# Performance work log

Measured on AMD Instinct MI355X. Metric: run time of the kernel, lower is better.

The kernel has to match this reference:

```python
import jax, jax.numpy as jnp
import numpy as np

B, S, D = 2, 2048, 2048
H, KVH, DH = 16, 4, 128
EPS = 1e-6
ROPE_BASE = 10000.0


def _rms_norm(x, eps=EPS):
    # weightless RMSNorm over the last (head) dim
    return x * jax.lax.rsqrt(jnp.mean(jnp.square(x), axis=-1, keepdims=True) + eps)


def _rope(x):
    # x: [b, s, h, d]; standard half-split RoPE, base 10000
    d = x.shape[-1]
    s = x.shape[1]
    inv_freq = 1.0 / (ROPE_BASE ** (jnp.arange(0, d // 2, dtype=jnp.float32) * 2.0 / d))
    ang = jnp.arange(s, dtype=jnp.float32)[:, None] * inv_freq[None, :]  # [s, d/2]
    cos = jnp.cos(ang)[None, :, None, :]
    sin = jnp.sin(ang)[None, :, None, :]
    x1, x2 = jnp.split(x, 2, axis=-1)
    return jnp.concatenate([x1 * cos - x2 * sin, x1 * sin + x2 * cos], axis=-1)


def setup_inputs() -> dict:
    key = jax.random.key(0)
    ks = jax.random.split(key, 5)
    x = jax.random.normal(ks[0], (B, S, D), dtype=jnp.float32)
    mask = jnp.tril(jnp.ones((S, S), dtype=bool))  # causal
    # eqx.Linear-style weights: [out, in], scaled init
    wq = jax.random.normal(ks[1], (D, D), dtype=jnp.float32) / np.sqrt(D)
    wk = jax.random.normal(ks[2], (KVH * DH, D), dtype=jnp.float32) / np.sqrt(D)
    wv = jax.random.normal(ks[3], (KVH * DH, D), dtype=jnp.float32) / np.sqrt(D)
    wo = jax.random.normal(ks[4], (D, D), dtype=jnp.float32) / np.sqrt(D)
    return {"x": x, "mask": mask, "wq": wq, "wk": wk, "wv": wv, "wo": wo}


def reference(x, mask, wq, wk, wv, wo):
    b, s, _ = x.shape
    q = jnp.einsum('bsi,oi->bso', x, wq).reshape(b, s, H, DH)
    k = jnp.einsum('bsi,oi->bso', x, wk).reshape(b, s, KVH, DH)
    v = jnp.einsum('bsi,oi->bso', x, wv).reshape(b, s, KVH, DH)
    rep = H // KVH
    k = jnp.repeat(k, rep, axis=-2)  # [b, s, H, DH]
    v = jnp.repeat(v, rep, axis=-2)
    q = _rms_norm(q)
    k = _rms_norm(k)
    q = _rope(q)
    k = _rope(k)
    scores = jnp.einsum('bshd,bthd->bhst', q, k) / jnp.sqrt(jnp.float32(DH))
    scores = jnp.where(mask[None, None], scores, -jnp.inf)
    w = jax.nn.softmax(scores, axis=-1)
    out = jnp.einsum('bhst,bthd->bshd', w, v).reshape(b, s, D)
    return jnp.einsum('bsi,oi->bso', out, wo)
```

## Files before the change

### kernel.cpp

```cpp
#include <hip/hip_runtime.h>
#include <hip/hip_bf16.h>

typedef unsigned short u16;
typedef unsigned int   u32;
typedef unsigned long long u64;
typedef __attribute__((ext_vector_type(8))) short bf16x8;
typedef __attribute__((ext_vector_type(4))) float f32x4;
typedef __attribute__((ext_vector_type(16))) float f32x16;

#define MFMA16(a,b,c) __builtin_amdgcn_mfma_f32_16x16x32_bf16((a),(b),(c),0,0,0)
#define MFMA32(a,b,c) __builtin_amdgcn_mfma_f32_32x32x16_bf16((a),(b),(c),0,0,0)

#define GLD16(gp, lp) __builtin_amdgcn_global_load_lds( \
    (const __attribute__((address_space(1))) void*)(gp), \
    (__attribute__((address_space(3))) void*)(lp), 16, 0, 0)

__device__ inline u32 pkbf(float a, float b) {
  __hip_bfloat16 ha = __float2bfloat16(a), hb = __float2bfloat16(b);
  return (u32)(*(u16*)&ha) | ((u32)(*(u16*)&hb) << 16);
}
__device__ inline float b2f(u16 x) {
  __hip_bfloat16 h; *(u16*)&h = x; return __bfloat162float(h);
}
__device__ inline u32 pk2(float a, float b) {
  u32 ua = __builtin_bit_cast(u32, a) + 0x8000u;
  u32 ub = __builtin_bit_cast(u32, b) + 0x8000u;
  return __builtin_amdgcn_perm(ub, ua, 0x07060302u);
}
__device__ inline float fmax3(float a, float b, float c) {
  return fmaxf(fmaxf(a, b), c);
}

__global__ __launch_bounds__(256) void cast_f32_bf16(const float* __restrict__ src,
                                                     u16* __restrict__ dst, int n4) {
  int i = blockIdx.x * 256 + threadIdx.x;
  if (i >= n4) return;
  float4 v = reinterpret_cast<const float4*>(src)[i];
  uint2 pk; pk.x = pkbf(v.x, v.y); pk.y = pkbf(v.z, v.w);
  reinterpret_cast<uint2*>(dst)[i] = pk;
}

__device__ inline void cstore(u16* C, size_t i, float v) {
  __hip_bfloat16 h = __float2bfloat16(v); C[i] = *(u16*)&h;
}
__device__ inline void cstore(float* C, size_t i, float v) { C[i] = v; }

template<typename OutT>
__global__ __launch_bounds__(512, 4) void gemm_big(const u16* __restrict__ A,
                                                   const u16* __restrict__ B,
                                                   OutT* __restrict__ C,
                                                   int M, int N, int K) {
  __shared__ u16 As[2][128 * 32];
  __shared__ u16 Bs[2][256 * 32];

  const int t = threadIdx.x;
  const int lane = t & 63, wid = t >> 6;
  const int l15 = lane & 15, l4 = lane >> 4;
  const int wr = wid >> 2, wc = wid & 3;

  const int nwg = gridDim.x * gridDim.y;
  int lid = blockIdx.y * gridDim.x + blockIdx.x;
  lid = (lid & 7) * (nwg >> 3) + (lid >> 3);
  const int m0 = (lid / gridDim.x) * 128, n0 = (lid % gridDim.x) * 256;

  const int ra = t >> 2;
  const int ca = (t & 3) ^ ((ra >> 1) & 3);
  const u16* Ag  = A + (size_t)(m0 + ra) * K + ca * 8;
  const u16* Bg0 = B + (size_t)(n0 + ra) * K + ca * 8;
  const u16* Bg1 = B + (size_t)(n0 + 128 + ra) * K + ca * 8;

#define STAGE(k0_, buf_) do {                                                 \
    GLD16(Ag  + (k0_), &As[buf_][t * 8]);                                     \
    GLD16(Bg0 + (k0_), &Bs[buf_][t * 8]);                                     \
    GLD16(Bg1 + (k0_), &Bs[buf_][4096 + t * 8]);                              \
  } while (0)

  const int nk = K >> 5;
  const int ks = (l15 >> 1) & 3;
  const int coff = ((l4 ^ ks) << 3);

  f32x4 acc[4][4] = {};

  STAGE(0, 0);
  STAGE(32, 1);

  for (int j = 0; j < nk; ++j) {
    const int cur = j & 1;
    if (j + 1 < nk) asm volatile("s_waitcnt vmcnt(3)" ::: "memory");
    else            asm volatile("s_waitcnt vmcnt(0)" ::: "memory");
    __builtin_amdgcn_s_barrier();
    __builtin_amdgcn_sched_barrier(0);

    bf16x8 af[4], bfr[4];
#pragma unroll
    for (int mi = 0; mi < 4; ++mi)
      af[mi] = *(const bf16x8*)&As[cur][(wr * 64 + mi * 16 + l15) * 32 + coff];
#pragma unroll
    for (int ni = 0; ni < 4; ++ni)
      bfr[ni] = *(const bf16x8*)&Bs[cur][(wc * 64 + ni * 16 + l15) * 32 + coff];
    __builtin_amdgcn_s_setprio(1);
#pragma unroll
    for (int mi = 0; mi < 4; ++mi)
#pragma unroll
      for (int ni = 0; ni < 4; ++ni)
        acc[mi][ni] = MFMA16(af[mi], bfr[ni], acc[mi][ni]);
    __builtin_amdgcn_s_setprio(0);

    __builtin_amdgcn_s_barrier();
    if (j + 2 < nk) STAGE((j + 2) << 5, cur);
  }

  const int crow = m0 + wr * 64 + (l4 << 2);
  const int ccol = n0 + wc * 64 + l15;
#pragma unroll
  for (int mi = 0; mi < 4; ++mi)
#pragma unroll
    for (int ni = 0; ni < 4; ++ni)
#pragma unroll
      for (int r = 0; r < 4; ++r)
        cstore(C, (size_t)(crow + mi * 16 + r) * N + (ccol + ni * 16), acc[mi][ni][r]);
#undef STAGE
}

__global__ __launch_bounds__(256) void rmsrope_kernel(u16* __restrict__ qkv) {
  const int t = threadIdx.x;
  const int lane = t & 63;
  const int gw = blockIdx.x * 4 + (t >> 6);
  const int row = gw / 20;
  const int hd = gw - row * 20;
  const int col = (hd < 16) ? hd * 128 : 2048 + (hd - 16) * 128;
  const size_t base = (size_t)row * 3072 + col;
  float x1 = b2f(qkv[base + lane]);
  float x2 = b2f(qkv[base + 64 + lane]);
  float ss = x1 * x1 + x2 * x2;
#pragma unroll
  for (int off = 32; off >= 1; off >>= 1) ss += __shfl_xor(ss, off, 64);
  const float qsc = (hd < 16) ? (0.08838834764831845f * 1.44269504088896340f)
                              : 1.0f;
  const float sc = rsqrtf(ss * (1.0f / 128.0f) + 1e-6f) * qsc;
  const int pos = row & 2047;
  const float inv_freq = exp2f(-(float)lane * (13.287712379549449f / 64.0f));
  float sn, cs;
  sincosf((float)pos * inv_freq, &sn, &cs);
  const float a = x1 * sc, b2 = x2 * sc;
  __hip_bfloat16 o1 = __float2bfloat16(a * cs - b2 * sn);
  __hip_bfloat16 o2 = __float2bfloat16(a * sn + b2 * cs);
  qkv[base + lane] = *(u16*)&o1;
  qkv[base + 64 + lane] = *(u16*)&o2;
}

__global__ __launch_bounds__(256) void vtrans_kernel(const u16* __restrict__ qkv,
                                                     u16* __restrict__ vt) {
  __shared__ u16 Ls[64 * 130];
  const int t = threadIdx.x;
  const int g = blockIdx.x & 7, sb = blockIdx.x >> 3;
  const int b = g >> 2, kvh = g & 3;
  const int vcol = 2560 + kvh * 128;
  {
    const int row = t >> 4, dch = t & 15;
    const u16* src = qkv + (size_t)(b * 2048 + sb * 64 + row) * 3072 + vcol + dch * 8;
#pragma unroll
    for (int it = 0; it < 4; ++it) {
      bf16x8 v = *(const bf16x8*)(src + (size_t)it * 16 * 3072);
      *(bf16x8*)&Ls[(row + it * 16) * 130 + dch * 8] = v;
    }
  }
  __syncthreads();
  const int c = t & 7, d0 = t >> 3;
  const int k0 = 4 * (8 * (c >> 2) + 4 * ((c >> 1) & 1) + (c & 1));
#pragma unroll
  for (int it = 0; it < 4; ++it) {
    const int d = d0 + 32 * it;
    u16 v[8];
#pragma unroll
    for (int e = 0; e < 8; ++e)
      v[e] = Ls[(k0 + (e & 3) + 8 * (e >> 2)) * 130 + d];
    u64 lo = (u64)v[0] | ((u64)v[1] << 16) | ((u64)v[2] << 32) | ((u64)v[3] << 48);
    u64 hi = (u64)v[4] | ((u64)v[5] << 16) | ((u64)v[6] << 32) | ((u64)v[7] << 48);
    u64* dst = (u64*)(vt + ((size_t)g * 128 + d) * 2048 + sb * 64 + c * 8);
    dst[0] = lo; dst[1] = hi;
  }
}

__global__ __launch_bounds__(256, 2) void attn_kernel(const u16* __restrict__ qkv,
                                                      const u16* __restrict__ vt,
                                                      u16* __restrict__ ao) {
  __shared__ u16 Ks[2][64 * 128];
  __shared__ u16 Vt[2][128 * 64];

  const int t = threadIdx.x;
  const int lane = t & 63, w = t >> 6;
  const int l31 = lane & 31, hi = lane >> 5;
  const int qg = w >> 1, hi2 = w & 1;

  const int bid = blockIdx.x;
  const int g = bid & 7;
  const int b = g >> 2, kvh = g & 3;
  const int idx = bid >> 3;
  const int h = kvh * 4 + (idx & 3);
  const int j = idx >> 2;

  const int kcol = 2048 + kvh * 128;
  const u16* vtg = vt + (size_t)g * 128 * 2048;

  const int krow_s = t >> 4, kchk = t & 15;
  const int vd = t >> 3, vc = t & 7;

#define STAGE_K(kb_, buf_) do {                                               \
    const size_t rb_ = (size_t)(b * 2048 + (kb_) * 64);                       \
    _Pragma("unroll")                                                         \
    for (int j_ = 0; j_ < 4; ++j_) {                                          \
      const int row_ = j_ * 16 + krow_s;                                      \
      GLD16(qkv + (rb_ + row_) * 3072 + kcol + ((kchk ^ (row_ & 7)) << 3),    \
            &Ks[buf_][(j_ * 256 + t) << 3]);                                  \
    } } while (0)

#define STAGE_V(kb_, buf_) do {                                               \
    _Pragma("unroll")                                                         \
    for (int j_ = 0; j_ < 4; ++j_) {                                          \
      const int d_ = j_ * 32 + vd;                                            \
      GLD16(vtg + (size_t)d_ * 2048 + (kb_) * 64 + ((vc ^ (d_ & 7)) << 3),    \
            &Vt[buf_][(j_ * 256 + t) << 3]);                                  \
    } } while (0)

  for (int ph = 0; ph < 2; ++ph) {
    const int qt64 = ph ? (31 - j) : j;
    const int q0 = qt64 * 64;
    const int nt = qt64 + 1;
    const int qrow = q0 + 32 * qg + l31;

    bf16x8 qf[8];
    {
      const u16* qp = qkv + (size_t)(b * 2048 + qrow) * 3072 + h * 128 + hi * 8;
#pragma unroll
      for (int st = 0; st < 8; ++st) qf[st] = *(const bf16x8*)(qp + st * 16);
    }

    f32x16 o[4];
#pragma unroll
    for (int dt = 0; dt < 4; ++dt)
#pragma unroll
      for (int i = 0; i < 16; ++i) o[dt][i] = 0.f;
    float m2 = -1e30f, l = 0.f;

    STAGE_K(0, 0);
    STAGE_V(0, 0);
    if (nt > 1) { STAGE_K(1, 1); STAGE_V(1, 1); }

    for (int kb = 0; kb < nt; ++kb) {
      const int cur = kb & 1;
      if (kb + 1 < nt) asm volatile("s_waitcnt vmcnt(8)" ::: "memory");
      else             asm volatile("s_waitcnt vmcnt(0)" ::: "memory");
      __builtin_amdgcn_s_barrier();
      __builtin_amdgcn_sched_barrier(0);

      f32x16 s;
#pragma unroll
      for (int i = 0; i < 16; ++i) s[i] = 0.f;
      const int kbase = (32 * hi2 + l31) * 128;
      const int ksw = l31 & 7;
      __builtin_amdgcn_s_setprio(1);
#pragma unroll
      for (int st = 0; st < 8; ++st) {
        bf16x8 ka = *(const bf16x8*)&Ks[cur][kbase + (((2 * st + hi) ^ ksw) << 3)];
        s = MFMA32(ka, qf[st], s);
      }
      __builtin_amdgcn_s_setprio(0);

      const bool nomask = (kb < qt64) || (hi2 == 0 && qg == 1);
      if (!nomask) {
#pragma unroll
        for (int i = 0; i < 16; ++i) {
          const int kr = kb * 64 + 32 * hi2 + (i & 3) + 8 * (i >> 2) + 4 * hi;
          s[i] = (kr <= qrow) ? s[i] : -INFINITY;
        }
      }
      float a0 = fmax3(s[0], s[1], s[2]);
      float a1 = fmax3(s[3], s[4], s[5]);
      float a2 = fmax3(s[6], s[7], s[8]);
      float a3 = fmax3(s[9], s[10], s[11]);
      float a4 = fmax3(s[12], s[13], s[14]);
      float b0 = fmax3(a0, a1, s[15]);
      float b1 = fmax3(a2, a3, a4);
      float pm = fmaxf(b0, b1);
      pm = fmaxf(pm, __shfl_xor(pm, 32));
      if (!__all(pm <= m2 + 8.f)) {
        const float m2n = fmaxf(m2, pm);
        const float fc = exp2f(m2 - m2n);
        m2 = m2n; l *= fc;
#pragma unroll
        for (int dt = 0; dt < 4; ++dt)
#pragma unroll
          for (int i = 0; i < 16; ++i) o[dt][i] *= fc;
      }
#pragma unroll
      for (int i = 0; i < 16; ++i) s[i] = exp2f(s[i] - m2);
      float t8[8];
#pragma unroll
      for (int i = 0; i < 8; ++i) t8[i] = s[i] + s[i + 8];
#pragma unroll
      for (int i = 0; i < 4; ++i) t8[i] = t8[i] + t8[i + 4];
      l += (t8[0] + t8[1]) + (t8[2] + t8[3]);
      union PB { u32 wd[4]; bf16x8 v; } p0u, p1u;
#pragma unroll
      for (int q_ = 0; q_ < 4; ++q_) {
        p0u.wd[q_] = pk2(s[2 * q_],     s[2 * q_ + 1]);
        p1u.wd[q_] = pk2(s[8 + 2 * q_], s[8 + 2 * q_ + 1]);
      }
      __builtin_amdgcn_s_setprio(1);
#pragma unroll
      for (int dt = 0; dt < 4; ++dt) {
        const int vrow = (dt * 32 + l31) * 64;
        const int dsw = l31 & 7;
        bf16x8 va0 = *(const bf16x8*)&Vt[cur][vrow + (((4 * hi2 + hi) ^ dsw) << 3)];
        o[dt] = MFMA32(va0, p0u.v, o[dt]);
        bf16x8 va1 = *(const bf16x8*)&Vt[cur][vrow + (((4 * hi2 + 2 + hi) ^ dsw) << 3)];
        o[dt] = MFMA32(va1, p1u.v, o[dt]);
      }
      __builtin_amdgcn_s_setprio(0);

      __builtin_amdgcn_s_barrier();
      if (kb + 2 < nt) { STAGE_K(kb + 2, cur); STAGE_V(kb + 2, cur); }
    }

    __syncthreads();
    const float l_tot = l + __shfl_xor(l, 32);
    float* Mrg = (float*)&Ks[0][0];
    float* Mlb = (float*)&Vt[0][0];
    const int sw8 = l31 & 7;
    if (hi2) {
#pragma unroll
      for (int dt = 0; dt < 4; ++dt) {
        const int rbase = ((qg * 4 + dt) * 32 + l31) * 32;
#pragma unroll
        for (int m_ = 0; m_ < 4; ++m_) {
          f32x4 cv;
          cv[0] = o[dt][4 * m_ + 0]; cv[1] = o[dt][4 * m_ + 1];
          cv[2] = o[dt][4 * m_ + 2]; cv[3] = o[dt][4 * m_ + 3];
          *(f32x4*)&Mrg[rbase + (((hi * 4 + m_) ^ sw8) << 2)] = cv;
        }
      }
      if (hi == 0) {
        Mlb[qg * 64 + l31] = m2;
        Mlb[qg * 64 + 32 + l31] = l_tot;
      }
    }
    __syncthreads();
    if (!hi2) {
      const float m1 = Mlb[qg * 64 + l31];
      const float l1 = Mlb[qg * 64 + 32 + l31];
      const float ms = fmaxf(m2, m1);
      const float w0 = exp2f(m2 - ms), w1 = exp2f(m1 - ms);
      const float inv = 1.f / (w0 * l_tot + w1 * l1);
      const float aw0 = w0 * inv, aw1 = w1 * inv;
      const size_t orow = (size_t)(b * 2048 + qrow) * 2048 + h * 128;
#pragma unroll
      for (int dt = 0; dt < 4; ++dt) {
        const int rbase = ((qg * 4 + dt) * 32 + l31) * 32;
#pragma unroll
        for (int m_ = 0; m_ < 4; ++m_) {
          f32x4 o1v = *(const f32x4*)&Mrg[rbase + (((hi * 4 + m_) ^ sw8) << 2)];
          u64 val = 0;
#pragma unroll
          for (int r = 0; r < 4; ++r) {
            __hip_bfloat16 hb =
                __float2bfloat16(aw0 * o[dt][4 * m_ + r] + aw1 * o1v[r]);
            val |= (u64)(*(u16*)&hb) << (16 * r);
          }
          *(u64*)&ao[orow + dt * 32 + 8 * m_ + 4 * hi] = val;
        }
      }
    }
    __syncthreads();
  }
#undef STAGE_K
#undef STAGE_V
}

extern "C" void kernel_launch(void* const* d_in, const int* in_sizes, int n_in,
                              void* d_out, int out_size, void* d_ws, size_t ws_size,
                              hipStream_t stream) {
  const float* x  = (const float*)d_in[0];
  const float* wq = (const float*)d_in[2];
  const float* wk = (const float*)d_in[3];
  const float* wv = (const float*)d_in[4];
  const float* wo = (const float*)d_in[5];
  float* out = (float*)d_out;

  u16* xb   = (u16*)d_ws;
  u16* wqkv = xb + (size_t)8388608;
  u16* qkv  = wqkv + (size_t)6291456;
  u16* vtg  = qkv + (size_t)12582912;
  u16* ao   = xb;
  u16* wob  = wqkv;

  cast_f32_bf16<<<8192, 256, 0, stream>>>(x,  xb,   2097152);
  cast_f32_bf16<<<4096, 256, 0, stream>>>(wq, wqkv, 1048576);
  cast_f32_bf16<<<1024, 256, 0, stream>>>(wk, wqkv + (size_t)4194304, 262144);
  cast_f32_bf16<<<1024, 256, 0, stream>>>(wv, wqkv + (size_t)5242880, 262144);

  gemm_big<u16><<<dim3(12, 32), 512, 0, stream>>>(xb, wqkv, qkv, 4096, 3072, 2048);

  cast_f32_bf16<<<4096, 256, 0, stream>>>(wo, wob, 1048576);

  rmsrope_kernel<<<20480, 256, 0, stream>>>(qkv);
  vtrans_kernel<<<256, 256, 0, stream>>>(qkv, vtg);

  attn_kernel<<<512, 256, 0, stream>>>(qkv, vtg, ao);

  gemm_big<float><<<dim3(8, 32), 512, 0, stream>>>(ao, wob, out, 4096, 2048, 2048);
}
```

Before: 218.7 us.

## Fuse casts into one kernel, use wider QKV GEMM tile, split attention MFMA chains

The five f32-to-bf16 cast launches become a single kernel that picks source and destination by index range, and the wo weight gets its own workspace slot so its cast can run up front. The QKV projection switches to a new GEMM with a 128x384 tile, giving a 256-block grid that matches the CU count, at the cost of more registers and lower occupancy. In attention, the QK^T reduction is split into two independent MFMA accumulator chains, and the V fragments are loaded from LDS before the softmax so LDS latency overlaps the exp math. This raises register pressure in the attention loop.

```diff
diff --git a/kernel.cpp b/kernel.cpp
--- a/kernel.cpp
+++ b/kernel.cpp
@@ -31,19 +31,110 @@
   return fmaxf(fmaxf(a, b), c);
 }
 
-__global__ __launch_bounds__(256) void cast_f32_bf16(const float* __restrict__ src,
-                                                     u16* __restrict__ dst, int n4) {
+__global__ __launch_bounds__(256) void cast_all(const float* __restrict__ x,
+                                                const float* __restrict__ wq,
+                                                const float* __restrict__ wk,
+                                                const float* __restrict__ wv,
+                                                const float* __restrict__ wo,
+                                                u16* __restrict__ xb,
+                                                u16* __restrict__ wqkv,
+                                                u16* __restrict__ wob) {
   int i = blockIdx.x * 256 + threadIdx.x;
-  if (i >= n4) return;
-  float4 v = reinterpret_cast<const float4*>(src)[i];
+  const float* src; u16* dst; int off;
+  if (i < 2097152)      { src = x;  dst = xb;                 off = 0; }
+  else if (i < 3145728) { src = wq; dst = wqkv;               off = 2097152; }
+  else if (i < 3407872) { src = wk; dst = wqkv + 4194304;     off = 3145728; }
+  else if (i < 3670016) { src = wv; dst = wqkv + 5242880;     off = 3407872; }
+  else                  { src = wo; dst = wob;                off = 3670016; }
+  const int k = i - off;
+  float4 v = reinterpret_cast<const float4*>(src)[k];
   uint2 pk; pk.x = pkbf(v.x, v.y); pk.y = pkbf(v.z, v.w);
-  reinterpret_cast<uint2*>(dst)[i] = pk;
+  reinterpret_cast<uint2*>(dst)[k] = pk;
 }
 
 __device__ inline void cstore(u16* C, size_t i, float v) {
   __hip_bfloat16 h = __float2bfloat16(v); C[i] = *(u16*)&h;
 }
 __device__ inline void cstore(float* C, size_t i, float v) { C[i] = v; }
+
+template<typename OutT>
+__global__ __launch_bounds__(512, 2) void gemm_wide(const u16* __restrict__ A,
+                                                    const u16* __restrict__ B,
+                                                    OutT* __restrict__ C,
+                                                    int M, int N, int K) {
+  __shared__ u16 As[2][128 * 32];
+  __shared__ u16 Bs[2][384 * 32];
+
+  const int t = threadIdx.x;
+  const int lane = t & 63, wid = t >> 6;
+  const int l15 = lane & 15, l4 = lane >> 4;
+  const int wr = wid >> 2, wc = wid & 3;
+
+  const int nwg = gridDim.x * gridDim.y;
+  int lid = blockIdx.y * gridDim.x + blockIdx.x;
+  lid = (lid & 7) * (nwg >> 3) + (lid >> 3);
+  const int m0 = (lid / gridDim.x) * 128, n0 = (lid % gridDim.x) * 384;
+
+  const int ra = t >> 2;
+  const int ca = (t & 3) ^ ((ra >> 1) & 3);
+  const u16* Ag  = A + (size_t)(m0 + ra) * K + ca * 8;
+  const u16* Bg0 = B + (size_t)(n0 + ra) * K + ca * 8;
+  const u16* Bg1 = B + (size_t)(n0 + 128 + ra) * K + ca * 8;
+  const u16* Bg2 = B + (size_t)(n0 + 256 + ra) * K + ca * 8;
+
+#define STAGE(k0_, buf_) do {                                                 \
+    GLD16(Ag  + (k0_), &As[buf_][t * 8]);                                     \
+    GLD16(Bg0 + (k0_), &Bs[buf_][t * 8]);                                     \
+    GLD16(Bg1 + (k0_), &Bs[buf_][4096 + t * 8]);                              \
+    GLD16(Bg2 + (k0_), &Bs[buf_][8192 + t * 8]);                              \
+  } while (0)
+
+  const int nk = K >> 5;
+  const int ks = (l15 >> 1) & 3;
+  const int coff = ((l4 ^ ks) << 3);
+
+  f32x4 acc[4][6] = {};
+
+  STAGE(0, 0);
+  STAGE(32, 1);
+
+  for (int j = 0; j < nk; ++j) {
+    const int cur = j & 1;
+    if (j + 1 < nk) asm volatile("s_waitcnt vmcnt(4)" ::: "memory");
+    else            asm volatile("s_waitcnt vmcnt(0)" ::: "memory");
+    __builtin_amdgcn_s_barrier();
+    __builtin_amdgcn_sched_barrier(0);
+
+    bf16x8 af[4], bfr[6];
+#pragma unroll
+    for (int mi = 0; mi < 4; ++mi)
+      af[mi] = *(const bf16x8*)&As[cur][(wr * 64 + mi * 16 + l15) * 32 + coff];
+#pragma unroll
+    for (int ni = 0; ni < 6; ++ni)
+      bfr[ni] = *(const bf16x8*)&Bs[cur][(wc * 96 + ni * 16 + l15) * 32 + coff];
+    __builtin_amdgcn_s_setprio(1);
+#pragma unroll
+    for (int mi = 0; mi < 4; ++mi)
+#pragma unroll
+      for (int ni = 0; ni < 6; ++ni)
+        acc[mi][ni] = MFMA16(af[mi], bfr[ni], acc[mi][ni]);
+    __builtin_amdgcn_s_setprio(0);
+
+    __builtin_amdgcn_s_barrier();
+    if (j + 2 < nk) STAGE((j + 2) << 5, cur);
+  }
+
+  const int crow = m0 + wr * 64 + (l4 << 2);
+  const int ccol = n0 + wc * 96 + l15;
+#pragma unroll
+  for (int mi = 0; mi < 4; ++mi)
+#pragma unroll
+    for (int ni = 0; ni < 6; ++ni)
+#pragma unroll
+      for (int r = 0; r < 4; ++r)
+        cstore(C, (size_t)(crow + mi * 16 + r) * N + (ccol + ni * 16), acc[mi][ni][r]);
+#undef STAGE
+}
 
 template<typename OutT>
 __global__ __launch_bounds__(512, 4) void gemm_big(const u16* __restrict__ A,
@@ -254,18 +345,31 @@
       __builtin_amdgcn_s_barrier();
       __builtin_amdgcn_sched_barrier(0);
 
-      f32x16 s;
-#pragma unroll
-      for (int i = 0; i < 16; ++i) s[i] = 0.f;
+      f32x16 sa, sb;
+#pragma unroll
+      for (int i = 0; i < 16; ++i) { sa[i] = 0.f; sb[i] = 0.f; }
       const int kbase = (32 * hi2 + l31) * 128;
       const int ksw = l31 & 7;
       __builtin_amdgcn_s_setprio(1);
 #pragma unroll
-      for (int st = 0; st < 8; ++st) {
+      for (int st = 0; st < 4; ++st) {
         bf16x8 ka = *(const bf16x8*)&Ks[cur][kbase + (((2 * st + hi) ^ ksw) << 3)];
-        s = MFMA32(ka, qf[st], s);
+        bf16x8 kb2 = *(const bf16x8*)&Ks[cur][kbase + (((2 * (st + 4) + hi) ^ ksw) << 3)];
+        sa = MFMA32(ka,  qf[st],     sa);
+        sb = MFMA32(kb2, qf[st + 4], sb);
       }
       __builtin_amdgcn_s_setprio(0);
+
+      bf16x8 va0[4], va1[4];
+#pragma unroll
+      for (int dt = 0; dt < 4; ++dt) {
+        const int vrow = (dt * 32 + l31) * 64;
+        const int dsw = l31 & 7;
+        va0[dt] = *(const bf16x8*)&Vt[cur][vrow + (((4 * hi2 + hi) ^ dsw) << 3)];
+        va1[dt] = *(const bf16x8*)&Vt[cur][vrow + (((4 * hi2 + 2 + hi) ^ dsw) << 3)];
+      }
+
+      f32x16 s = sa + sb;
 
       const bool nomask = (kb < qt64) || (hi2 == 0 && qg == 1);
       if (!nomask) {
@@ -310,12 +414,8 @@
       __builtin_amdgcn_s_setprio(1);
 #pragma unroll
       for (int dt = 0; dt < 4; ++dt) {
-        const int vrow = (dt * 32 + l31) * 64;
-        const int dsw = l31 & 7;
-        bf16x8 va0 = *(const bf16x8*)&Vt[cur][vrow + (((4 * hi2 + hi) ^ dsw) << 3)];
-        o[dt] = MFMA32(va0, p0u.v, o[dt]);
-        bf16x8 va1 = *(const bf16x8*)&Vt[cur][vrow + (((4 * hi2 + 2 + hi) ^ dsw) << 3)];
-        o[dt] = MFMA32(va1, p1u.v, o[dt]);
+        o[dt] = MFMA32(va0[dt], p0u.v, o[dt]);
+        o[dt] = MFMA32(va1[dt], p1u.v, o[dt]);
       }
       __builtin_amdgcn_s_setprio(0);
 
@@ -391,17 +491,12 @@
   u16* wqkv = xb + (size_t)8388608;
   u16* qkv  = wqkv + (size_t)6291456;
   u16* vtg  = qkv + (size_t)12582912;
+  u16* wob  = vtg + (size_t)2097152;
   u16* ao   = xb;
-  u16* wob  = wqkv;
-
-  cast_f32_bf16<<<8192, 256, 0, stream>>>(x,  xb,   2097152);
-  cast_f32_bf16<<<4096, 256, 0, stream>>>(wq, wqkv, 1048576);
-  cast_f32_bf16<<<1024, 256, 0, stream>>>(wk, wqkv + (size_t)4194304, 262144);
-  cast_f32_bf16<<<1024, 256, 0, stream>>>(wv, wqkv + (size_t)5242880, 262144);
-
-  gemm_big<u16><<<dim3(12, 32), 512, 0, stream>>>(xb, wqkv, qkv, 4096, 3072, 2048);
-
-  cast_f32_bf16<<<4096, 256, 0, stream>>>(wo, wob, 1048576);
+
+  cast_all<<<18432, 256, 0, stream>>>(x, wq, wk, wv, wo, xb, wqkv, wob);
+
+  gemm_wide<u16><<<dim3(8, 32), 512, 0, stream>>>(xb, wqkv, qkv, 4096, 3072, 2048);
 
   rmsrope_kernel<<<20480, 256, 0, stream>>>(qkv);
   vtrans_kernel<<<256, 256, 0, stream>>>(qkv, vtg);
```

Measured after the change: 226.6 us. 1.04x slower.
